# Kernel tuning notes

Hardware: AMD Instinct MI355X
Metric: run time of the kernel (lower is better)

## Reference

```python
import jax, jax.numpy as jnp
import numpy as np
import math

B, T, C, H, D = 4, 2048, 1024, 16, 64  # batch, seq, n_embd, n_head, head_dim


def setup_inputs() -> dict:
    key = jax.random.key(0)
    kx, kq, kk, kv, ko = jax.random.split(key, 5)
    x = jax.random.normal(kx, (B, T, C), dtype=jnp.float32)
    # standard RoPE tables, half head_dim
    d = D // 2
    inv_freq = 1.0 / (10000.0 ** (jnp.arange(d, dtype=jnp.float32) / d))
    freqs = jnp.outer(jnp.arange(T, dtype=jnp.float32), inv_freq)  # [T, d]
    cos = jnp.cos(freqs)[None, None]  # [1,1,T,d]
    sin = jnp.sin(freqs)[None, None]
    s = 0.02
    Wq = jax.random.normal(kq, (C, C), dtype=jnp.float32) * s  # stored [in,out]
    Wk = jax.random.normal(kk, (C, C), dtype=jnp.float32) * s
    Wv = jax.random.normal(kv, (C, C), dtype=jnp.float32) * s
    Wo = jax.random.normal(ko, (C, C), dtype=jnp.float32) * s
    return {"x": x, "cos": cos, "sin": sin, "Wq": Wq, "Wk": Wk, "Wv": Wv, "Wo": Wo}


def _rope(u, cos, sin):
    # u: [B,H,T,D]; rotate-half style RoPE matching apply_rotary_emb
    d = u.shape[-1] // 2
    u1, u2 = u[..., :d], u[..., d:]
    return jnp.concatenate([u1 * cos + u2 * sin, -u1 * sin + u2 * cos], axis=-1)


def _rms_norm(u):
    # parameter-free RMSNorm, eps = finfo eps (torch F.rms_norm default)
    eps = jnp.finfo(u.dtype).eps
    return u * jax.lax.rsqrt(jnp.mean(u * u, axis=-1, keepdims=True) + eps)


def reference(x, cos, sin, Wq, Wk, Wv, Wo):
    b, t, c = x.shape

    def split_heads(h):
        return h.reshape(b, t, H, D).transpose(0, 2, 1, 3)  # [B,H,T,D]

    q = split_heads(x @ Wq)
    k = split_heads(x @ Wk)
    v = split_heads(x @ Wv)
    q = _rms_norm(_rope(q, cos, sin))
    k = _rms_norm(_rope(k, cos, sin))
    scale = 1.0 / math.sqrt(D)
    scores = jnp.einsum('bhqd,bhkd->bhqk', q, k) * scale  # [B,H,T,T]
    causal = jnp.tril(jnp.ones((t, t), dtype=bool))
    scores = jnp.where(causal, scores, -jnp.inf)
    attn = jax.nn.softmax(scores, axis=-1)
    y = jnp.einsum('bhqk,bhkd->bhqd', attn, v)
    y = y.transpose(0, 2, 1, 3).reshape(b, t, c)
    return y @ Wo
```

## Files before the change

kernel.cpp:

```cpp
#include <hip/hip_runtime.h>


typedef __attribute__((ext_vector_type(8))) short short8;
typedef __attribute__((ext_vector_type(4))) short short4v;
typedef __attribute__((ext_vector_type(4))) float f32x4;

__device__ __forceinline__ unsigned short f2b(float f) {
  union { float f; unsigned int i; } x; x.f = f;
  return (unsigned short)((x.i + 0x7FFFu + ((x.i >> 16) & 1u)) >> 16);
}

__device__ __forceinline__ unsigned short b16(float f) {
  return __builtin_bit_cast(unsigned short, (__bf16)f);
}

__device__ __forceinline__ void glds16(const void* g, void* l) {
  __builtin_amdgcn_global_load_lds((const __attribute__((address_space(1))) unsigned int*)g,
                                   (__attribute__((address_space(3))) unsigned int*)l,
                                   16, 0, 0);
}

__device__ __forceinline__ f32x4 mfma16(short8 a, short8 b, f32x4 c) {
  return __builtin_amdgcn_mfma_f32_16x16x32_bf16(a, b, c, 0, 0, 0);
}

__global__ __launch_bounds__(256) void cast_x_kernel(const float* __restrict__ x,
                                                     unsigned short* __restrict__ xb) {
  const long i = ((long)blockIdx.x * 256 + threadIdx.x) * 8;
  const float4 a = *(const float4*)(x + i);
  const float4 b = *(const float4*)(x + i + 4);
  unsigned short o[8] = {f2b(a.x), f2b(a.y), f2b(a.z), f2b(a.w),
                         f2b(b.x), f2b(b.y), f2b(b.z), f2b(b.w)};
  *(short8*)(xb + i) = *(const short8*)o;
}

__global__ __launch_bounds__(256) void transpose_cast_w(
    const float* __restrict__ W0, const float* __restrict__ W1,
    const float* __restrict__ W2, const float* __restrict__ W3,
    unsigned short* __restrict__ Wt, unsigned short* __restrict__ Wot) {
  const int z = blockIdx.z;
  const float* __restrict__ W = (z == 0) ? W0 : (z == 1) ? W1 : (z == 2) ? W2 : W3;
  unsigned short* __restrict__ dst = (z < 3) ? (Wt + (size_t)z * 1024 * 1024) : Wot;
  __shared__ float tile[32][33];
  const int tx = threadIdx.x, ty = threadIdx.y;
  const int bx = blockIdx.x * 32, by = blockIdx.y * 32;
#pragma unroll
  for (int i = 0; i < 4; ++i)
    tile[ty + 8 * i][tx] = W[(size_t)(by + ty + 8 * i) * 1024 + bx + tx];
  __syncthreads();
#pragma unroll
  for (int i = 0; i < 4; ++i)
    dst[(size_t)(bx + ty + 8 * i) * 1024 + by + tx] = f2b(tile[tx][ty + 8 * i]);
}

__global__ __launch_bounds__(256) void gemm_qkv(
    const unsigned short* __restrict__ A, const unsigned short* __restrict__ Bt,
    unsigned short* __restrict__ Qr, unsigned short* __restrict__ Kr,
    unsigned short* __restrict__ Vr,
    const float* __restrict__ cosp, const float* __restrict__ sinp) {
  __shared__ unsigned short As[128 * 32];
  __shared__ unsigned short Bs[128 * 32];
  const int tid = threadIdx.x;
  const int wave = tid >> 6, lane = tid & 63;
  const int ln = lane & 15, grp = lane >> 4;
  const int wr = wave >> 1, wc = wave & 1;
  const int row0 = blockIdx.x * 128, col0 = blockIdx.y * 128;

  f32x4 acc[4][4];
  const f32x4 z4 = {0.f, 0.f, 0.f, 0.f};
#pragma unroll
  for (int m = 0; m < 4; ++m)
#pragma unroll
    for (int n = 0; n < 4; ++n) acc[m][n] = z4;

  for (int k0 = 0; k0 < 1024; k0 += 32) {
    __syncthreads();
#pragma unroll
    for (int p = 0; p < 2; ++p) {
      const int lin = p * 256 + tid;
      const int r = lin >> 2;
      const int c8 = (lin & 3) * 8;
      glds16(A + (long)(row0 + r) * 1024 + k0 + c8, (char*)As + p * 4096 + wave * 1024);
      glds16(Bt + (long)(col0 + r) * 1024 + k0 + c8, (char*)Bs + p * 4096 + wave * 1024);
    }
    __syncthreads();
    short8 af[4], bfv[4];
#pragma unroll
    for (int m = 0; m < 4; ++m)
      af[m] = *(const short8*)&As[(wr * 64 + m * 16 + ln) * 32 + grp * 8];
#pragma unroll
    for (int n = 0; n < 4; ++n)
      bfv[n] = *(const short8*)&Bs[(wc * 64 + n * 16 + ln) * 32 + grp * 8];
#pragma unroll
    for (int m = 0; m < 4; ++m)
#pragma unroll
      for (int n = 0; n < 4; ++n)
        acc[m][n] = mfma16(af[m], bfv[n], acc[m][n]);
  }

  const int colbase = col0 + wc * 64;
  const int z = colbase >> 10;
  const int h = (colbase & 1023) >> 6;
  unsigned short* __restrict__ dst = (z == 0) ? Qr : (z == 1) ? Kr : Vr;

  if (z < 2) {
    const float qs = (z == 0) ? 0.125f * 1.44269504f : 1.0f;
#pragma unroll
    for (int m = 0; m < 4; ++m) {
#pragma unroll
      for (int reg = 0; reg < 4; ++reg) {
        const int row = row0 + wr * 64 + m * 16 + grp * 4 + reg;
        const int t = row & 2047, b = row >> 11;
        const float u0 = acc[m][0][reg], u1 = acc[m][1][reg];
        const float u2 = acc[m][2][reg], u3 = acc[m][3][reg];
        const float c0 = cosp[t * 32 + ln],      s0 = sinp[t * 32 + ln];
        const float c1 = cosp[t * 32 + 16 + ln], s1 = sinp[t * 32 + 16 + ln];
        const float r0 =  u0 * c0 + u2 * s0;
        const float r1 =  u1 * c1 + u3 * s1;
        const float r2 = -u0 * s0 + u2 * c0;
        const float r3 = -u1 * s1 + u3 * c1;
        float ss = r0 * r0 + r1 * r1 + r2 * r2 + r3 * r3;
        ss += __shfl_xor(ss, 1); ss += __shfl_xor(ss, 2);
        ss += __shfl_xor(ss, 4); ss += __shfl_xor(ss, 8);
        const float inv = rsqrtf(ss * (1.0f / 64.0f) + 1.1920929e-07f) * qs;
        const long base = (((long)(b * 16 + h)) * 2048 + t) * 64;
        dst[base + ln]      = f2b(r0 * inv);
        dst[base + 16 + ln] = f2b(r1 * inv);
        dst[base + 32 + ln] = f2b(r2 * inv);
        dst[base + 48 + ln] = f2b(r3 * inv);
      }
    }
  } else {
#pragma unroll
    for (int m = 0; m < 4; ++m) {
#pragma unroll
      for (int reg = 0; reg < 4; ++reg) {
        const int row = row0 + wr * 64 + m * 16 + grp * 4 + reg;
        const int t = row & 2047, b = row >> 11;
        const long base = (((long)(b * 16 + h)) * 2048 + t) * 64;
#pragma unroll
        for (int n = 0; n < 4; ++n)
          dst[base + n * 16 + ln] = f2b(acc[m][n][reg]);
      }
    }
  }
}

__global__ __launch_bounds__(256) void attn_kernel(
    const unsigned short* __restrict__ Q, const unsigned short* __restrict__ K,
    const unsigned short* __restrict__ V, unsigned short* __restrict__ Y) {
  __shared__ unsigned short lds[2 * 8192];
  const int tid = threadIdx.x;
  const int wave = tid >> 6, lane = tid & 63;
  const int ln = lane & 15, grp = lane >> 4;

  const int linb = blockIdx.x;
  const int xcd = linb & 7, slot = linb >> 3;
  const int bh = xcd * 8 + (slot >> 3);
  const int pr = slot & 7;

  const long bhT = (long)bh * 2048;
  const int b = bh >> 4, h = bh & 15;
  auto* lds3 = (__attribute__((address_space(3))) unsigned short*)lds;

  auto stage = [&](int j, int buf) {
    const long kvoff = bhT + (long)j * 64;
    char* Kb = (char*)lds + buf * 16384;
#pragma unroll
    for (int p = 0; p < 2; ++p) {
      const int cl = p * 256 + tid;
      const int krow = cl >> 3;
      const int kcb = ((cl & 7) * 16) ^ ((krow & 7) << 4);
      glds16(K + (kvoff + krow) * 64 + (kcb >> 1), Kb + p * 4096 + wave * 1024);
      const int dtv = cl >> 7, kvt = (cl >> 3) & 15, rr = (cl >> 1) & 3, hf = cl & 1;
      glds16(V + (kvoff + kvt * 4 + rr) * 64 + dtv * 16 + hf * 8,
             Kb + 8192 + p * 4096 + wave * 1024);
    }
  };

  const f32x4 z4 = {0.f, 0.f, 0.f, 0.f};

  for (int half = 0; half < 2; ++half) {
    const int bx = (half == 0) ? pr : 15 - pr;
    const int q0 = bx * 128;
    const int qw = q0 + wave * 32;
    const int jmax = 2 * bx + 1;
    const int jdiag = 2 * bx;

    short8 qf[2][2];
#pragma unroll
    for (int nt = 0; nt < 2; ++nt)
#pragma unroll
      for (int c = 0; c < 2; ++c)
        qf[nt][c] = *(const short8*)(Q + (bhT + qw + nt * 16 + ln) * 64 + c * 32 + grp * 8);

    f32x4 accO[4][2];
#pragma unroll
    for (int dt = 0; dt < 4; ++dt) { accO[dt][0] = z4; accO[dt][1] = z4; }
    float m_run[2] = {-INFINITY, -INFINITY};
    float l_run[2] = {0.f, 0.f};

    stage(0, 0);
    asm volatile("s_waitcnt vmcnt(0)" ::: "memory");
    __builtin_amdgcn_s_barrier();

    int cur = 0;
    for (int j = 0; j <= jmax; ++j, cur ^= 1) {
      if (j < jmax) {
        stage(j + 1, cur ^ 1);
        asm volatile("s_waitcnt vmcnt(4)" ::: "memory");
      } else {
        asm volatile("s_waitcnt vmcnt(0)" ::: "memory");
      }
      __builtin_amdgcn_s_barrier();

      const unsigned short* Kb = lds + cur * 8192;
      const bool maskp = (j >= jdiag);

      f32x4 sacc[4][2];
#pragma unroll
      for (int ct = 0; ct < 4; ++ct) { sacc[ct][0] = z4; sacc[ct][1] = z4; }
      __builtin_amdgcn_s_setprio(1);
#pragma unroll
      for (int ct = 0; ct < 4; ++ct) {
        const int row = ct * 16 + ln;
        const int sw = (ln & 7) << 4;
        const char* rp = (const char*)Kb + row * 128;
        const short8 kf0 = *(const short8*)(rp + ((grp * 16) ^ sw));
        const short8 kf1 = *(const short8*)(rp + ((grp * 16 + 64) ^ sw));
        sacc[ct][0] = mfma16(kf0, qf[0][0], sacc[ct][0]);
        sacc[ct][0] = mfma16(kf1, qf[0][1], sacc[ct][0]);
        sacc[ct][1] = mfma16(kf0, qf[1][0], sacc[ct][1]);
        sacc[ct][1] = mfma16(kf1, qf[1][1], sacc[ct][1]);
      }
      __builtin_amdgcn_s_setprio(0);

      short8 pf[2][2];
#pragma unroll
      for (int nt = 0; nt < 2; ++nt) {
        if (maskp) {
          const int q = qw + nt * 16 + ln;
#pragma unroll
          for (int ct = 0; ct < 4; ++ct)
#pragma unroll
            for (int r = 0; r < 4; ++r) {
              const int kv = j * 64 + ct * 16 + grp * 4 + r;
              if (kv > q) sacc[ct][nt][r] = -INFINITY;
            }
        }
        float mx = sacc[0][nt][0];
#pragma unroll
        for (int ct = 0; ct < 4; ++ct)
#pragma unroll
          for (int r = 0; r < 4; ++r) mx = fmaxf(mx, sacc[ct][nt][r]);
        mx = fmaxf(mx, __shfl_xor(mx, 16));
        mx = fmaxf(mx, __shfl_xor(mx, 32));
        if (!__all(mx - m_run[nt] <= 8.f)) {
          const float mnew = fmaxf(m_run[nt], mx);
          const float alpha = exp2f(m_run[nt] - mnew);
          m_run[nt] = mnew;
          l_run[nt] *= alpha;
#pragma unroll
          for (int dt = 0; dt < 4; ++dt) accO[dt][nt] *= alpha;
        }
        float rs = 0.f;
#pragma unroll
        for (int ct = 0; ct < 4; ++ct)
#pragma unroll
          for (int r = 0; r < 4; ++r) {
            const float p = exp2f(sacc[ct][nt][r] - m_run[nt]);
            rs += p;
            pf[nt][ct >> 1][(ct & 1) * 4 + r] = (short)b16(p);
          }
        rs += __shfl_xor(rs, 16);
        rs += __shfl_xor(rs, 32);
        l_run[nt] += rs;
      }

      const unsigned vb = (unsigned)(size_t)&lds3[cur * 8192 + 4096] + (unsigned)lane * 8;
      short4v t[4][4];
#pragma unroll
      for (int dt = 0; dt < 4; ++dt) {
        const unsigned va = vb + dt * 2048;
        asm volatile("ds_read_b64_tr_b16 %0, %4 offset:0\n\t"
                     "ds_read_b64_tr_b16 %1, %4 offset:512\n\t"
                     "ds_read_b64_tr_b16 %2, %4 offset:1024\n\t"
                     "ds_read_b64_tr_b16 %3, %4 offset:1536"
                     : "=&v"(t[dt][0]), "=&v"(t[dt][1]), "=&v"(t[dt][2]), "=&v"(t[dt][3])
                     : "v"(va));
      }
      asm volatile("s_waitcnt lgkmcnt(0)" ::: "memory");
      __builtin_amdgcn_sched_barrier(0);
      __builtin_amdgcn_s_setprio(1);
#pragma unroll
      for (int dt = 0; dt < 4; ++dt) {
        const short8 vf0 = __builtin_shufflevector(t[dt][0], t[dt][1], 0, 1, 2, 3, 4, 5, 6, 7);
        const short8 vf1 = __builtin_shufflevector(t[dt][2], t[dt][3], 0, 1, 2, 3, 4, 5, 6, 7);
        accO[dt][0] = mfma16(vf0, pf[0][0], accO[dt][0]);
        accO[dt][0] = mfma16(vf1, pf[0][1], accO[dt][0]);
        accO[dt][1] = mfma16(vf0, pf[1][0], accO[dt][1]);
        accO[dt][1] = mfma16(vf1, pf[1][1], accO[dt][1]);
      }
      __builtin_amdgcn_s_setprio(0);
      asm volatile("s_waitcnt lgkmcnt(0)" ::: "memory");
      __builtin_amdgcn_s_barrier();
    }

#pragma unroll
    for (int nt = 0; nt < 2; ++nt) {
      const float inv = 1.0f / l_run[nt];
      const int t_ = qw + nt * 16 + ln;
      const long base = (((long)(b * 2048 + t_)) * 16 + h) * 64;
#pragma unroll
      for (int dt = 0; dt < 4; ++dt) {
        unsigned short o[4];
#pragma unroll
        for (int r = 0; r < 4; ++r) o[r] = b16(accO[dt][nt][r] * inv);
        *(short4v*)(Y + base + dt * 16 + grp * 4) = *(const short4v*)o;
      }
    }
  }
}

__global__ __launch_bounds__(256) void gemm_out(
    const unsigned short* __restrict__ A, const unsigned short* __restrict__ Bt,
    float* __restrict__ C) {
  __shared__ unsigned short As[128 * 32];
  __shared__ unsigned short Bs[128 * 32];
  const int tid = threadIdx.x;
  const int wave = tid >> 6, lane = tid & 63;
  const int ln = lane & 15, grp = lane >> 4;
  const int wr = wave >> 1, wc = wave & 1;
  const int row0 = blockIdx.x * 128, col0 = blockIdx.y * 128;

  f32x4 acc[4][4];
  const f32x4 z4 = {0.f, 0.f, 0.f, 0.f};
#pragma unroll
  for (int m = 0; m < 4; ++m)
#pragma unroll
    for (int n = 0; n < 4; ++n) acc[m][n] = z4;

  for (int k0 = 0; k0 < 1024; k0 += 32) {
    __syncthreads();
#pragma unroll
    for (int p = 0; p < 2; ++p) {
      const int lin = p * 256 + tid;
      const int r = lin >> 2;
      const int c8 = (lin & 3) * 8;
      glds16(A + (long)(row0 + r) * 1024 + k0 + c8, (char*)As + p * 4096 + wave * 1024);
      glds16(Bt + (long)(col0 + r) * 1024 + k0 + c8, (char*)Bs + p * 4096 + wave * 1024);
    }
    __syncthreads();
    short8 af[4], bfv[4];
#pragma unroll
    for (int m = 0; m < 4; ++m)
      af[m] = *(const short8*)&As[(wr * 64 + m * 16 + ln) * 32 + grp * 8];
#pragma unroll
    for (int n = 0; n < 4; ++n)
      bfv[n] = *(const short8*)&Bs[(wc * 64 + n * 16 + ln) * 32 + grp * 8];
#pragma unroll
    for (int m = 0; m < 4; ++m)
#pragma unroll
      for (int n = 0; n < 4; ++n)
        acc[m][n] = mfma16(af[m], bfv[n], acc[m][n]);
  }

#pragma unroll
  for (int m = 0; m < 4; ++m)
#pragma unroll
    for (int reg = 0; reg < 4; ++reg) {
      const int row = row0 + wr * 64 + m * 16 + grp * 4 + reg;
#pragma unroll
      for (int n = 0; n < 4; ++n)
        C[(long)row * 1024 + col0 + wc * 64 + n * 16 + ln] = acc[m][n][reg];
    }
}

extern "C" void kernel_launch(void* const* d_in, const int* in_sizes, int n_in,
                              void* d_out, int out_size, void* d_ws, size_t ws_size,
                              hipStream_t stream) {
  (void)in_sizes; (void)n_in; (void)out_size; (void)ws_size;
  const float* x    = (const float*)d_in[0];
  const float* cosp = (const float*)d_in[1];
  const float* sinp = (const float*)d_in[2];
  const float* Wq   = (const float*)d_in[3];
  const float* Wk   = (const float*)d_in[4];
  const float* Wv   = (const float*)d_in[5];
  const float* Wo   = (const float*)d_in[6];
  float* out = (float*)d_out;

  unsigned short* xb  = (unsigned short*)d_ws;
  unsigned short* Wt  = xb  + (size_t)8192 * 1024;
  unsigned short* Wot = Wt  + (size_t)3 * 1024 * 1024;
  unsigned short* Qr  = Wot + (size_t)1024 * 1024;
  unsigned short* Kr  = Qr  + (size_t)8192 * 1024;
  unsigned short* Vr  = Kr  + (size_t)8192 * 1024;
  unsigned short* Yb  = xb;

  cast_x_kernel<<<4096, 256, 0, stream>>>(x, xb);
  transpose_cast_w<<<dim3(32, 32, 4), dim3(32, 8), 0, stream>>>(Wq, Wk, Wv, Wo, Wt, Wot);
  gemm_qkv<<<dim3(64, 24), 256, 0, stream>>>(xb, Wt, Qr, Kr, Vr, cosp, sinp);
  attn_kernel<<<512, 256, 0, stream>>>(Qr, Kr, Vr, Yb);
  gemm_out<<<dim3(64, 8), 256, 0, stream>>>(Yb, Wot, out);
}
```

Baseline: 205.9 us.

## Double attention KV tile size to 128 keys per iteration

Changes the flash-attention inner loop to process 128 keys per iteration instead of 64. LDS staging doubles to 64KB, and the causal mask now applies only on the last tile. The V transpose reads are interleaved per d-tile with the PV MFMAs rather than all issued up front. This halves the per-iteration barrier and softmax-rescale overhead, at the cost of more registers, more LDS (lower occupancy) and more masked work on the diagonal tile.

```diff
diff --git a/kernel.cpp b/kernel.cpp
--- a/kernel.cpp
+++ b/kernel.cpp
@@ -149,7 +149,7 @@
 __global__ __launch_bounds__(256) void attn_kernel(
     const unsigned short* __restrict__ Q, const unsigned short* __restrict__ K,
     const unsigned short* __restrict__ V, unsigned short* __restrict__ Y) {
-  __shared__ unsigned short lds[2 * 8192];
+  __shared__ unsigned short lds[2 * 16384];
   const int tid = threadIdx.x;
   const int wave = tid >> 6, lane = tid & 63;
   const int ln = lane & 15, grp = lane >> 4;
@@ -164,17 +164,17 @@
   auto* lds3 = (__attribute__((address_space(3))) unsigned short*)lds;
 
   auto stage = [&](int j, int buf) {
-    const long kvoff = bhT + (long)j * 64;
-    char* Kb = (char*)lds + buf * 16384;
-#pragma unroll
-    for (int p = 0; p < 2; ++p) {
+    const long kvoff = bhT + (long)j * 128;
+    char* Kb = (char*)lds + buf * 32768;
+#pragma unroll
+    for (int p = 0; p < 4; ++p) {
       const int cl = p * 256 + tid;
       const int krow = cl >> 3;
       const int kcb = ((cl & 7) * 16) ^ ((krow & 7) << 4);
       glds16(K + (kvoff + krow) * 64 + (kcb >> 1), Kb + p * 4096 + wave * 1024);
-      const int dtv = cl >> 7, kvt = (cl >> 3) & 15, rr = (cl >> 1) & 3, hf = cl & 1;
+      const int dtv = cl >> 8, kvt = (cl >> 3) & 31, rr = (cl >> 1) & 3, hf = cl & 1;
       glds16(V + (kvoff + kvt * 4 + rr) * 64 + dtv * 16 + hf * 8,
-             Kb + 8192 + p * 4096 + wave * 1024);
+             Kb + 16384 + p * 4096 + wave * 1024);
     }
   };
 
@@ -182,10 +182,8 @@
 
   for (int half = 0; half < 2; ++half) {
     const int bx = (half == 0) ? pr : 15 - pr;
-    const int q0 = bx * 128;
-    const int qw = q0 + wave * 32;
-    const int jmax = 2 * bx + 1;
-    const int jdiag = 2 * bx;
+    const int qw = bx * 128 + wave * 32;
+    const int jmax = bx;
 
     short8 qf[2][2];
 #pragma unroll
@@ -208,21 +206,21 @@
     for (int j = 0; j <= jmax; ++j, cur ^= 1) {
       if (j < jmax) {
         stage(j + 1, cur ^ 1);
-        asm volatile("s_waitcnt vmcnt(4)" ::: "memory");
+        asm volatile("s_waitcnt vmcnt(8)" ::: "memory");
       } else {
         asm volatile("s_waitcnt vmcnt(0)" ::: "memory");
       }
       __builtin_amdgcn_s_barrier();
 
-      const unsigned short* Kb = lds + cur * 8192;
-      const bool maskp = (j >= jdiag);
-
-      f32x4 sacc[4][2];
-#pragma unroll
-      for (int ct = 0; ct < 4; ++ct) { sacc[ct][0] = z4; sacc[ct][1] = z4; }
+      const unsigned short* Kb = lds + cur * 16384;
+      const bool maskp = (j == jmax);
+
+      f32x4 sacc[8][2];
+#pragma unroll
+      for (int ct = 0; ct < 8; ++ct) { sacc[ct][0] = z4; sacc[ct][1] = z4; }
       __builtin_amdgcn_s_setprio(1);
 #pragma unroll
-      for (int ct = 0; ct < 4; ++ct) {
+      for (int ct = 0; ct < 8; ++ct) {
         const int row = ct * 16 + ln;
         const int sw = (ln & 7) << 4;
         const char* rp = (const char*)Kb + row * 128;
@@ -235,22 +233,22 @@
       }
       __builtin_amdgcn_s_setprio(0);
 
-      short8 pf[2][2];
+      short8 pf[2][4];
 #pragma unroll
       for (int nt = 0; nt < 2; ++nt) {
         if (maskp) {
           const int q = qw + nt * 16 + ln;
 #pragma unroll
-          for (int ct = 0; ct < 4; ++ct)
+          for (int ct = 0; ct < 8; ++ct)
 #pragma unroll
             for (int r = 0; r < 4; ++r) {
-              const int kv = j * 64 + ct * 16 + grp * 4 + r;
+              const int kv = j * 128 + ct * 16 + grp * 4 + r;
               if (kv > q) sacc[ct][nt][r] = -INFINITY;
             }
         }
         float mx = sacc[0][nt][0];
 #pragma unroll
-        for (int ct = 0; ct < 4; ++ct)
+        for (int ct = 0; ct < 8; ++ct)
 #pragma unroll
           for (int r = 0; r < 4; ++r) mx = fmaxf(mx, sacc[ct][nt][r]);
         mx = fmaxf(mx, __shfl_xor(mx, 16));
@@ -265,7 +263,7 @@
         }
         float rs = 0.f;
 #pragma unroll
-        for (int ct = 0; ct < 4; ++ct)
+        for (int ct = 0; ct < 8; ++ct)
 #pragma unroll
           for (int r = 0; r < 4; ++r) {
             const float p = exp2f(sacc[ct][nt][r] - m_run[nt]);
@@ -277,32 +275,40 @@
         l_run[nt] += rs;
       }
 
-      const unsigned vb = (unsigned)(size_t)&lds3[cur * 8192 + 4096] + (unsigned)lane * 8;
-      short4v t[4][4];
+      const unsigned vb = (unsigned)(size_t)&lds3[cur * 16384 + 8192] + (unsigned)lane * 8;
+      __builtin_amdgcn_s_setprio(1);
 #pragma unroll
       for (int dt = 0; dt < 4; ++dt) {
-        const unsigned va = vb + dt * 2048;
+        const unsigned va = vb + dt * 4096;
+        short4v t0, t1, t2, t3, t4, t5, t6, t7;
         asm volatile("ds_read_b64_tr_b16 %0, %4 offset:0\n\t"
                      "ds_read_b64_tr_b16 %1, %4 offset:512\n\t"
                      "ds_read_b64_tr_b16 %2, %4 offset:1024\n\t"
                      "ds_read_b64_tr_b16 %3, %4 offset:1536"
-                     : "=&v"(t[dt][0]), "=&v"(t[dt][1]), "=&v"(t[dt][2]), "=&v"(t[dt][3])
+                     : "=&v"(t0), "=&v"(t1), "=&v"(t2), "=&v"(t3)
                      : "v"(va));
-      }
-      asm volatile("s_waitcnt lgkmcnt(0)" ::: "memory");
-      __builtin_amdgcn_sched_barrier(0);
-      __builtin_amdgcn_s_setprio(1);
-#pragma unroll
-      for (int dt = 0; dt < 4; ++dt) {
-        const short8 vf0 = __builtin_shufflevector(t[dt][0], t[dt][1], 0, 1, 2, 3, 4, 5, 6, 7);
-        const short8 vf1 = __builtin_shufflevector(t[dt][2], t[dt][3], 0, 1, 2, 3, 4, 5, 6, 7);
+        asm volatile("ds_read_b64_tr_b16 %0, %4 offset:2048\n\t"
+                     "ds_read_b64_tr_b16 %1, %4 offset:2560\n\t"
+                     "ds_read_b64_tr_b16 %2, %4 offset:3072\n\t"
+                     "ds_read_b64_tr_b16 %3, %4 offset:3584"
+                     : "=&v"(t4), "=&v"(t5), "=&v"(t6), "=&v"(t7)
+                     : "v"(va));
+        asm volatile("s_waitcnt lgkmcnt(0)" ::: "memory");
+        __builtin_amdgcn_sched_barrier(0);
+        const short8 vf0 = __builtin_shufflevector(t0, t1, 0, 1, 2, 3, 4, 5, 6, 7);
+        const short8 vf1 = __builtin_shufflevector(t2, t3, 0, 1, 2, 3, 4, 5, 6, 7);
+        const short8 vf2 = __builtin_shufflevector(t4, t5, 0, 1, 2, 3, 4, 5, 6, 7);
+        const short8 vf3 = __builtin_shufflevector(t6, t7, 0, 1, 2, 3, 4, 5, 6, 7);
         accO[dt][0] = mfma16(vf0, pf[0][0], accO[dt][0]);
         accO[dt][0] = mfma16(vf1, pf[0][1], accO[dt][0]);
+        accO[dt][0] = mfma16(vf2, pf[0][2], accO[dt][0]);
+        accO[dt][0] = mfma16(vf3, pf[0][3], accO[dt][0]);
         accO[dt][1] = mfma16(vf0, pf[1][0], accO[dt][1]);
         accO[dt][1] = mfma16(vf1, pf[1][1], accO[dt][1]);
+        accO[dt][1] = mfma16(vf2, pf[1][2], accO[dt][1]);
+        accO[dt][1] = mfma16(vf3, pf[1][3], accO[dt][1]);
       }
       __builtin_amdgcn_s_setprio(0);
-      asm volatile("s_waitcnt lgkmcnt(0)" ::: "memory");
       __builtin_amdgcn_s_barrier();
     }
 
```

Result: slower. 226.8 us (+10.2%).

## Halve attention query tile to 64 rows and double grid size

Applied to the files above, without the earlier changes.

The attention kernel now gives each block a 64-row query tile, each wave handling 16 query rows, instead of 128 rows with 32 per wave. The grid doubles to 1024 blocks with a paired causal schedule over 32 tiles. This is meant to raise occupancy and balance work across CUs, and it cuts per-wave registers. In exchange, each K/V tile loaded into LDS is reused by half as many queries, so LDS staging traffic and barriers per unit of compute roughly double. A redundant lgkmcnt wait before the end-of-iteration barrier is also removed.

```diff
diff --git a/kernel.cpp b/kernel.cpp
--- a/kernel.cpp
+++ b/kernel.cpp
@@ -156,8 +156,8 @@
 
   const int linb = blockIdx.x;
   const int xcd = linb & 7, slot = linb >> 3;
-  const int bh = xcd * 8 + (slot >> 3);
-  const int pr = slot & 7;
+  const int bh = xcd * 8 + (slot >> 4);
+  const int pr = slot & 15;
 
   const long bhT = (long)bh * 2048;
   const int b = bh >> 4, h = bh & 15;
@@ -181,24 +181,20 @@
   const f32x4 z4 = {0.f, 0.f, 0.f, 0.f};
 
   for (int half = 0; half < 2; ++half) {
-    const int bx = (half == 0) ? pr : 15 - pr;
-    const int q0 = bx * 128;
-    const int qw = q0 + wave * 32;
-    const int jmax = 2 * bx + 1;
-    const int jdiag = 2 * bx;
-
-    short8 qf[2][2];
-#pragma unroll
-    for (int nt = 0; nt < 2; ++nt)
-#pragma unroll
-      for (int c = 0; c < 2; ++c)
-        qf[nt][c] = *(const short8*)(Q + (bhT + qw + nt * 16 + ln) * 64 + c * 32 + grp * 8);
-
-    f32x4 accO[4][2];
-#pragma unroll
-    for (int dt = 0; dt < 4; ++dt) { accO[dt][0] = z4; accO[dt][1] = z4; }
-    float m_run[2] = {-INFINITY, -INFINITY};
-    float l_run[2] = {0.f, 0.f};
+    const int bx = (half == 0) ? pr : 31 - pr;
+    const int qw = bx * 64 + wave * 16;
+    const int jmax = bx;
+
+    short8 qf[2];
+#pragma unroll
+    for (int c = 0; c < 2; ++c)
+      qf[c] = *(const short8*)(Q + (bhT + qw + ln) * 64 + c * 32 + grp * 8);
+
+    f32x4 accO[4];
+#pragma unroll
+    for (int dt = 0; dt < 4; ++dt) accO[dt] = z4;
+    float m_run = -INFINITY;
+    float l_run = 0.f;
 
     stage(0, 0);
     asm volatile("s_waitcnt vmcnt(0)" ::: "memory");
@@ -215,11 +211,11 @@
       __builtin_amdgcn_s_barrier();
 
       const unsigned short* Kb = lds + cur * 8192;
-      const bool maskp = (j >= jdiag);
-
-      f32x4 sacc[4][2];
-#pragma unroll
-      for (int ct = 0; ct < 4; ++ct) { sacc[ct][0] = z4; sacc[ct][1] = z4; }
+      const bool maskp = (j == jmax);
+
+      f32x4 sacc[4];
+#pragma unroll
+      for (int ct = 0; ct < 4; ++ct) sacc[ct] = z4;
       __builtin_amdgcn_s_setprio(1);
 #pragma unroll
       for (int ct = 0; ct < 4; ++ct) {
@@ -228,53 +224,50 @@
         const char* rp = (const char*)Kb + row * 128;
         const short8 kf0 = *(const short8*)(rp + ((grp * 16) ^ sw));
         const short8 kf1 = *(const short8*)(rp + ((grp * 16 + 64) ^ sw));
-        sacc[ct][0] = mfma16(kf0, qf[0][0], sacc[ct][0]);
-        sacc[ct][0] = mfma16(kf1, qf[0][1], sacc[ct][0]);
-        sacc[ct][1] = mfma16(kf0, qf[1][0], sacc[ct][1]);
-        sacc[ct][1] = mfma16(kf1, qf[1][1], sacc[ct][1]);
+        sacc[ct] = mfma16(kf0, qf[0], sacc[ct]);
+        sacc[ct] = mfma16(kf1, qf[1], sacc[ct]);
       }
       __builtin_amdgcn_s_setprio(0);
 
-      short8 pf[2][2];
-#pragma unroll
-      for (int nt = 0; nt < 2; ++nt) {
+      short8 pf[2];
+      {
         if (maskp) {
-          const int q = qw + nt * 16 + ln;
+          const int q = qw + ln;
 #pragma unroll
           for (int ct = 0; ct < 4; ++ct)
 #pragma unroll
             for (int r = 0; r < 4; ++r) {
               const int kv = j * 64 + ct * 16 + grp * 4 + r;
-              if (kv > q) sacc[ct][nt][r] = -INFINITY;
+              if (kv > q) sacc[ct][r] = -INFINITY;
             }
         }
-        float mx = sacc[0][nt][0];
+        float mx = sacc[0][0];
 #pragma unroll
         for (int ct = 0; ct < 4; ++ct)
 #pragma unroll
-          for (int r = 0; r < 4; ++r) mx = fmaxf(mx, sacc[ct][nt][r]);
+          for (int r = 0; r < 4; ++r) mx = fmaxf(mx, sacc[ct][r]);
         mx = fmaxf(mx, __shfl_xor(mx, 16));
         mx = fmaxf(mx, __shfl_xor(mx, 32));
-        if (!__all(mx - m_run[nt] <= 8.f)) {
-          const float mnew = fmaxf(m_run[nt], mx);
-          const float alpha = exp2f(m_run[nt] - mnew);
-          m_run[nt] = mnew;
-          l_run[nt] *= alpha;
-#pragma unroll
-          for (int dt = 0; dt < 4; ++dt) accO[dt][nt] *= alpha;
+        if (!__all(mx - m_run <= 8.f)) {
+          const float mnew = fmaxf(m_run, mx);
+          const float alpha = exp2f(m_run - mnew);
+          m_run = mnew;
+          l_run *= alpha;
+#pragma unroll
+          for (int dt = 0; dt < 4; ++dt) accO[dt] *= alpha;
         }
         float rs = 0.f;
 #pragma unroll
         for (int ct = 0; ct < 4; ++ct)
 #pragma unroll
           for (int r = 0; r < 4; ++r) {
-            const float p = exp2f(sacc[ct][nt][r] - m_run[nt]);
+            const float p = exp2f(sacc[ct][r] - m_run);
             rs += p;
-            pf[nt][ct >> 1][(ct & 1) * 4 + r] = (short)b16(p);
+            pf[ct >> 1][(ct & 1) * 4 + r] = (short)b16(p);
           }
         rs += __shfl_xor(rs, 16);
         rs += __shfl_xor(rs, 32);
-        l_run[nt] += rs;
+        l_run += rs;
       }
 
       const unsigned vb = (unsigned)(size_t)&lds3[cur * 8192 + 4096] + (unsigned)lane * 8;
@@ -296,26 +289,22 @@
       for (int dt = 0; dt < 4; ++dt) {
         const short8 vf0 = __builtin_shufflevector(t[dt][0], t[dt][1], 0, 1, 2, 3, 4, 5, 6, 7);
         const short8 vf1 = __builtin_shufflevector(t[dt][2], t[dt][3], 0, 1, 2, 3, 4, 5, 6, 7);
-        accO[dt][0] = mfma16(vf0, pf[0][0], accO[dt][0]);
-        accO[dt][0] = mfma16(vf1, pf[0][1], accO[dt][0]);
-        accO[dt][1] = mfma16(vf0, pf[1][0], accO[dt][1]);
-        accO[dt][1] = mfma16(vf1, pf[1][1], accO[dt][1]);
+        accO[dt] = mfma16(vf0, pf[0], accO[dt]);
+        accO[dt] = mfma16(vf1, pf[1], accO[dt]);
       }
       __builtin_amdgcn_s_setprio(0);
-      asm volatile("s_waitcnt lgkmcnt(0)" ::: "memory");
       __builtin_amdgcn_s_barrier();
     }
 
-#pragma unroll
-    for (int nt = 0; nt < 2; ++nt) {
-      const float inv = 1.0f / l_run[nt];
-      const int t_ = qw + nt * 16 + ln;
+    {
+      const float inv = 1.0f / l_run;
+      const int t_ = qw + ln;
       const long base = (((long)(b * 2048 + t_)) * 16 + h) * 64;
 #pragma unroll
       for (int dt = 0; dt < 4; ++dt) {
         unsigned short o[4];
 #pragma unroll
-        for (int r = 0; r < 4; ++r) o[r] = b16(accO[dt][nt][r] * inv);
+        for (int r = 0; r < 4; ++r) o[r] = b16(accO[dt][r] * inv);
         *(short4v*)(Y + base + dt * 16 + grp * 4) = *(const short4v*)o;
       }
     }
@@ -400,6 +389,6 @@
   cast_x_kernel<<<4096, 256, 0, stream>>>(x, xb);
   transpose_cast_w<<<dim3(32, 32, 4), dim3(32, 8), 0, stream>>>(Wq, Wk, Wv, Wo, Wt, Wot);
   gemm_qkv<<<dim3(64, 24), 256, 0, stream>>>(xb, Wt, Qr, Kr, Vr, cosp, sinp);
-  attn_kernel<<<512, 256, 0, stream>>>(Qr, Kr, Vr, Yb);
+  attn_kernel<<<1024, 256, 0, stream>>>(Qr, Kr, Vr, Yb);
   gemm_out<<<dim3(64, 8), 256, 0, stream>>>(Yb, Wot, out);
 }
```

After: 199.8 us. -2.9%, faster.
